# Optimization experiments

Hardware: AMD Instinct MI355X
Metric: run time of the kernel (lower is better)

The kernel has to match this reference:

```python
import jax, jax.numpy as jnp
import numpy as np

INIT_RANGE = 0.02

def setup_inputs() -> dict:
    key = jax.random.key(0)
    ks = jax.random.split(key, 5)
    B, S, D, H, Dh = 4, 2048, 768, 12, 64
    residual = jax.random.normal(ks[0], (B, S, D), dtype=jnp.float32)
    W_Q = jax.random.normal(ks[1], (H, D, Dh), dtype=jnp.float32) * INIT_RANGE
    W_K = jax.random.normal(ks[2], (H, D, Dh), dtype=jnp.float32) * INIT_RANGE
    W_V = jax.random.normal(ks[3], (H, D, Dh), dtype=jnp.float32) * INIT_RANGE
    W_O = jax.random.normal(ks[4], (H, Dh, D), dtype=jnp.float32) * INIT_RANGE
    b_Q = jnp.zeros((H, Dh), dtype=jnp.float32)
    b_K = jnp.zeros((H, Dh), dtype=jnp.float32)
    b_V = jnp.zeros((H, Dh), dtype=jnp.float32)
    b_O = jnp.zeros((D,), dtype=jnp.float32)
    return {"residual": residual, "W_Q": W_Q, "W_K": W_K, "W_V": W_V,
            "W_O": W_O, "b_Q": b_Q, "b_K": b_K, "b_V": b_V, "b_O": b_O}

def reference(residual, W_Q, W_K, W_V, W_O, b_Q, b_K, b_V, b_O):
    # residual: [b, s, d]; W_{Q,K,V}: [h, d, dh]; W_O: [h, dh, d]
    d_head = W_Q.shape[-1]
    q = jnp.einsum('bsd,hde->bshe', residual, W_Q) + b_Q  # [b, s, h, dh]
    k = jnp.einsum('bsd,hde->bshe', residual, W_K) + b_K
    v = jnp.einsum('bsd,hde->bshe', residual, W_V) + b_V
    scores = jnp.einsum('bqhe,bkhe->bhqk', q, k) / jnp.sqrt(jnp.float32(d_head))
    S = residual.shape[1]
    causal = jnp.tril(jnp.ones((S, S), dtype=bool))  # True where attending allowed
    scores = jnp.where(causal, scores, -jnp.inf)
    pattern = jax.nn.softmax(scores, axis=-1)  # [b, h, q, k]
    z = jnp.einsum('bkhe,bhqk->bqhe', v, pattern)  # [b, q, h, dh]
    attn_out = jnp.einsum('bqhe,hed->bqd', z, W_O) + b_O
    return attn_out
```

## Files before the change

kernel.cpp:

```cpp
#include <hip/hip_runtime.h>

typedef short short8 __attribute__((ext_vector_type(8)));
typedef float floatx4 __attribute__((ext_vector_type(4)));
typedef unsigned short ushort_t;


__device__ inline ushort_t f2bf(float f) {
  union { float f; unsigned u; } x; x.f = f;
  unsigned u = x.u;
  unsigned r = u + 0x7fffu + ((u >> 16) & 1u);
  return (ushort_t)(r >> 16);
}

__device__ inline unsigned pk2(float a, float b) {
  union { float f; unsigned u; } x, y; x.f = a; y.f = b;
  return ((x.u + 0x8000u) >> 16) | ((y.u + 0x8000u) & 0xffff0000u);
}

__device__ inline float fexp2(float x) {
#if __has_builtin(__builtin_amdgcn_exp2f)
  return __builtin_amdgcn_exp2f(x);
#else
  return exp2f(x);
#endif
}

__device__ inline void async16(const void* g, void* l) {
  __builtin_amdgcn_global_load_lds((const __attribute__((address_space(1))) void*)g,
                                   (__attribute__((address_space(3))) void*)l,
                                   16, 0, 0);
}


__global__ __launch_bounds__(256) void conv_rx(const float* __restrict__ x,
                                               ushort_t* __restrict__ y, int n4) {
  int i = blockIdx.x * 256 + threadIdx.x;
  if (i >= n4) return;
  float4 f = ((const float4*)x)[i];
  ushort4 o;
  o.x = f2bf(f.x); o.y = f2bf(f.y); o.z = f2bf(f.z); o.w = f2bf(f.w);
  ((ushort4*)y)[i] = o;
}

__global__ __launch_bounds__(256) void conv_w2(
    const float* __restrict__ wq, const float* __restrict__ wk, const float* __restrict__ wv,
    const float* __restrict__ wo,
    const float* __restrict__ bq, const float* __restrict__ bk, const float* __restrict__ bv,
    ushort_t* __restrict__ wqkvT, ushort_t* __restrict__ woT, float* __restrict__ bqkv)
{
  __shared__ ushort_t t[64 * 72];
  const int bid = blockIdx.x;
  const int tid = threadIdx.x;
  if (bid < 432) {
    int m = bid / 144, rem = bid % 144;
    int h = rem / 12, dt = rem % 12;
    int d0 = dt * 64;
    const float* w = (m == 0) ? wq : ((m == 1) ? wk : wv);
    const float* src = w + ((size_t)h * 768 + d0) * 64;
#pragma unroll
    for (int i = 0; i < 4; ++i) {
      int task = i * 256 + tid;
      int row = task >> 4, c4 = task & 15;
      float4 f = *(const float4*)(src + row * 64 + c4 * 4);
      ushort4 o4;
      o4.x = f2bf(f.x); o4.y = f2bf(f.y); o4.z = f2bf(f.z); o4.w = f2bf(f.w);
      *(ushort4*)&t[row * 72 + c4 * 4] = o4;
    }
    __syncthreads();
    ushort_t* dst = wqkvT + ((size_t)m * 768 + h * 64) * 768 + d0;
#pragma unroll
    for (int i = 0; i < 2; ++i) {
      int task = i * 256 + tid;
      int e = task >> 3, sc = task & 7;
      short8 d8;
#pragma unroll
      for (int j = 0; j < 8; ++j) d8[j] = (short)t[(sc * 8 + j) * 72 + e];
      *(short8*)(dst + (size_t)e * 768 + sc * 8) = d8;
    }
  } else if (bid < 576) {
    int b2 = bid - 432;
    int het = b2 / 12, dt = b2 % 12;
    int he0 = het * 64, d0 = dt * 64;
    const float* src = wo + (size_t)he0 * 768 + d0;
#pragma unroll
    for (int i = 0; i < 4; ++i) {
      int task = i * 256 + tid;
      int row = task >> 4, c4 = task & 15;
      float4 f = *(const float4*)(src + (size_t)row * 768 + c4 * 4);
      ushort4 o4;
      o4.x = f2bf(f.x); o4.y = f2bf(f.y); o4.z = f2bf(f.z); o4.w = f2bf(f.w);
      *(ushort4*)&t[row * 72 + c4 * 4] = o4;
    }
    __syncthreads();
    ushort_t* dst = woT + (size_t)d0 * 768 + he0;
#pragma unroll
    for (int i = 0; i < 2; ++i) {
      int task = i * 256 + tid;
      int dd = task >> 3, sc = task & 7;
      short8 d8;
#pragma unroll
      for (int j = 0; j < 8; ++j) d8[j] = (short)t[(sc * 8 + j) * 72 + dd];
      *(short8*)(dst + (size_t)dd * 768 + sc * 8) = d8;
    }
  } else {
    for (int idx = tid; idx < 2304; idx += 256) {
      int m = idx / 768, rem = idx - m * 768;
      const float* bp = (m == 0) ? bq : ((m == 1) ? bk : bv);
      bqkv[idx] = bp[rem];
    }
  }
}


__global__ __launch_bounds__(256) void gemm_qkv(
    const ushort_t* __restrict__ A, const ushort_t* __restrict__ Bt,
    const float* __restrict__ bias,
    ushort_t* __restrict__ q, ushort_t* __restrict__ k, ushort_t* __restrict__ v)
{
  __shared__ ushort_t lA[2][128 * 32];
  __shared__ ushort_t lB[2][128 * 32];
  const int tid = threadIdx.x;
  const int wave = tid >> 6, lane = tid & 63;
  const int ln15 = lane & 15, quad = lane >> 4;
  const int row0 = blockIdx.x * 128, col0 = blockIdx.y * 128;
  const int wm = (wave >> 1) * 64, wn = (wave & 1) * 64;
  const int c0 = wave * 2;

  const ushort_t* gA0 = A + (size_t)(row0 + c0 * 16 + (lane >> 2)) * 768 + (lane & 3) * 8;
  const ushort_t* gB0 = Bt + (size_t)(col0 + c0 * 16 + (lane >> 2)) * 768 + (lane & 3) * 8;

  floatx4 acc[4][4];
#pragma unroll
  for (int mi = 0; mi < 4; ++mi)
#pragma unroll
    for (int ni = 0; ni < 4; ++ni)
      acc[mi][ni] = (floatx4){0.f, 0.f, 0.f, 0.f};

  async16(gA0, &lA[0][c0 * 512]);
  async16(gA0 + 16 * 768, &lA[0][c0 * 512 + 512]);
  async16(gB0, &lB[0][c0 * 512]);
  async16(gB0 + 16 * 768, &lB[0][c0 * 512 + 512]);
  __syncthreads();

  for (int kt = 0; kt < 24; ++kt) {
    const int buf = kt & 1;
    if (kt + 1 < 24) {
      async16(gA0 + (kt + 1) * 32, &lA[buf ^ 1][c0 * 512]);
      async16(gA0 + (kt + 1) * 32 + 16 * 768, &lA[buf ^ 1][c0 * 512 + 512]);
      async16(gB0 + (kt + 1) * 32, &lB[buf ^ 1][c0 * 512]);
      async16(gB0 + (kt + 1) * 32 + 16 * 768, &lB[buf ^ 1][c0 * 512 + 512]);
    }
    short8 af[4], bfv[4];
#pragma unroll
    for (int mi = 0; mi < 4; ++mi)
      af[mi] = *(const short8*)&lA[buf][(wm + mi * 16 + ln15) * 32 + quad * 8];
#pragma unroll
    for (int ni = 0; ni < 4; ++ni)
      bfv[ni] = *(const short8*)&lB[buf][(wn + ni * 16 + ln15) * 32 + quad * 8];
#pragma unroll
    for (int mi = 0; mi < 4; ++mi)
#pragma unroll
      for (int ni = 0; ni < 4; ++ni)
        acc[mi][ni] = __builtin_amdgcn_mfma_f32_16x16x32_bf16(af[mi], bfv[ni], acc[mi][ni], 0, 0, 0);
    __syncthreads();
  }

  const float qscale = 0.125f * 1.44269504f;
#pragma unroll
  for (int mi = 0; mi < 4; ++mi) {
#pragma unroll
    for (int ni = 0; ni < 4; ++ni) {
      int gr = row0 + wm + mi * 16 + quad * 4;
      int gc = col0 + wn + ni * 16 + ln15;
      float bia = bias[gc];
      int m = gc / 768;
      int rem = gc - m * 768;
      int h = rem >> 6, e = rem & 63;
      ushort_t* dp = (m == 0) ? q : ((m == 1) ? k : v);
#pragma unroll
      for (int r = 0; r < 4; ++r) {
        float val = acc[mi][ni][r] + bia;
        int rr = gr + r;
        int bb = rr >> 11, ss = rr & 2047;
        size_t dst = ((size_t)((bb * 12 + h) * 2048 + ss) << 6) + e;
        dp[dst] = f2bf((m == 0) ? val * qscale : val);
      }
    }
  }
}


__global__ __launch_bounds__(256) void gemm_out(
    const ushort_t* __restrict__ A, const ushort_t* __restrict__ Bt,
    const float* __restrict__ bias, float* __restrict__ outf)
{
  __shared__ ushort_t lA[2][64 * 32];
  __shared__ ushort_t lB[2][128 * 32];
  const int tid = threadIdx.x;
  const int wave = tid >> 6, lane = tid & 63;
  const int ln15 = lane & 15, quad = lane >> 4;
  const int row0 = blockIdx.x * 64, col0 = blockIdx.y * 128;
  const int wm = (wave >> 1) * 32, wn = (wave & 1) * 64;
  const int cb = wave * 2;

  const ushort_t* gA0 = A + (size_t)(row0 + wave * 16 + (lane >> 2)) * 768 + (lane & 3) * 8;
  const ushort_t* gB0 = Bt + (size_t)(col0 + cb * 16 + (lane >> 2)) * 768 + (lane & 3) * 8;

  floatx4 acc[2][4];
#pragma unroll
  for (int mi = 0; mi < 2; ++mi)
#pragma unroll
    for (int ni = 0; ni < 4; ++ni)
      acc[mi][ni] = (floatx4){0.f, 0.f, 0.f, 0.f};

  async16(gA0, &lA[0][wave * 512]);
  async16(gB0, &lB[0][cb * 512]);
  async16(gB0 + 16 * 768, &lB[0][cb * 512 + 512]);
  __syncthreads();

  for (int kt = 0; kt < 24; ++kt) {
    const int buf = kt & 1;
    if (kt + 1 < 24) {
      async16(gA0 + (kt + 1) * 32, &lA[buf ^ 1][wave * 512]);
      async16(gB0 + (kt + 1) * 32, &lB[buf ^ 1][cb * 512]);
      async16(gB0 + (kt + 1) * 32 + 16 * 768, &lB[buf ^ 1][cb * 512 + 512]);
    }
    short8 af[2], bfv[4];
#pragma unroll
    for (int mi = 0; mi < 2; ++mi)
      af[mi] = *(const short8*)&lA[buf][(wm + mi * 16 + ln15) * 32 + quad * 8];
#pragma unroll
    for (int ni = 0; ni < 4; ++ni)
      bfv[ni] = *(const short8*)&lB[buf][(wn + ni * 16 + ln15) * 32 + quad * 8];
#pragma unroll
    for (int mi = 0; mi < 2; ++mi)
#pragma unroll
      for (int ni = 0; ni < 4; ++ni)
        acc[mi][ni] = __builtin_amdgcn_mfma_f32_16x16x32_bf16(af[mi], bfv[ni], acc[mi][ni], 0, 0, 0);
    __syncthreads();
  }

#pragma unroll
  for (int mi = 0; mi < 2; ++mi) {
#pragma unroll
    for (int ni = 0; ni < 4; ++ni) {
      int gr = row0 + wm + mi * 16 + quad * 4;
      int gc = col0 + wn + ni * 16 + ln15;
      float bia = bias[gc];
#pragma unroll
      for (int r = 0; r < 4; ++r)
        outf[(size_t)(gr + r) * 768 + gc] = acc[mi][ni][r] + bia;
    }
  }
}


__global__ __launch_bounds__(256) void transpose_v(const ushort_t* __restrict__ v,
                                                   ushort_t* __restrict__ vt)
{
  __shared__ ushort_t t[64 * 72];
  const int bh = blockIdx.y;
  const int s0 = blockIdx.x * 64;
  const ushort_t* src = v + ((size_t)bh * 2048 + s0) * 64;
#pragma unroll
  for (int t2 = 0; t2 < 2; ++t2) {
    int task = t2 * 256 + threadIdx.x;
    int row = task >> 3, ch = task & 7;
    short8 d = *(const short8*)(src + row * 64 + ch * 8);
    *(short8*)&t[row * 72 + ch * 8] = d;
  }
  __syncthreads();
  ushort_t* dst = vt + (size_t)bh * 64 * 2048 + s0;
#pragma unroll
  for (int t2 = 0; t2 < 2; ++t2) {
    int task = t2 * 256 + threadIdx.x;
    int e = task >> 3, sc = task & 7;
    short8 d;
#pragma unroll
    for (int j = 0; j < 8; ++j)
      d[j] = (short)t[(sc * 8 + j) * 72 + e];
    *(short8*)(dst + (size_t)e * 2048 + sc * 8) = d;
  }
}


__device__ inline short8 frag_ld(const ushort_t* t, int row, int ch) {
  return *(const short8*)&t[row * 64 + (((ch ^ row) & 7) * 8)];
}

__global__ __launch_bounds__(256) void attn3(
    const ushort_t* __restrict__ Q, const ushort_t* __restrict__ K,
    const ushort_t* __restrict__ VT, ushort_t* __restrict__ Z)
{
  __shared__ ushort_t lK[2][64 * 64];
  __shared__ ushort_t lV[2][64 * 64];
  __shared__ ushort_t lPQ[128 * 64];
  const int tid = threadIdx.x;
  const int wave = tid >> 6, lane = tid & 63;
  const int ln15 = lane & 15, quad = lane >> 4;
  const int bi = blockIdx.x;
  const int bh = bi % 48;
  const int t = 15 - (bi / 48);
  const int h = bh % 12, b = bh / 12;
  const size_t base = (size_t)bh * 2048 * 64;
  const ushort_t* Qp = Q + base + (size_t)t * 128 * 64;
  const ushort_t* Kp = K + base;
  const ushort_t* Vp = VT + base;
  const int nk = 2 * t + 2;

#pragma unroll
  for (int i = 0; i < 4; ++i) {
    int task = i * 256 + tid;
    int row = task >> 3, lch = task & 7;
    int c = lch ^ (row & 7);
    async16(Qp + row * 64 + c * 8, &lPQ[task * 8]);
  }
#pragma unroll
  for (int i = 0; i < 2; ++i) {
    int task = i * 256 + tid;
    int row = task >> 3, lch = task & 7;
    int c = lch ^ (row & 7);
    async16(Kp + (size_t)row * 64 + c * 8, &lK[0][task * 8]);
    async16(Vp + (size_t)row * 2048 + c * 8, &lV[0][task * 8]);
  }
  __syncthreads();
  short8 qf[2][2];
#pragma unroll
  for (int c = 0; c < 2; ++c) {
    qf[c][0] = frag_ld(lPQ, wave * 32 + c * 16 + ln15, quad);
    qf[c][1] = frag_ld(lPQ, wave * 32 + c * 16 + ln15, quad + 4);
  }
  __syncthreads();

  float l_i[2] = {0.f, 0.f};
  floatx4 o[2][4];
#pragma unroll
  for (int c = 0; c < 2; ++c)
#pragma unroll
    for (int et = 0; et < 4; ++et) o[c][et] = (floatx4){0.f, 0.f, 0.f, 0.f};

  ushort_t* lPw = lPQ + wave * 2048;
  const int qg0 = t * 128 + wave * 32 + ln15;

  for (int kt = 0; kt < nk; ++kt) {
    const int buf = kt & 1;
    if (kt + 1 < nk) {
#pragma unroll
      for (int i = 0; i < 2; ++i) {
        int task = i * 256 + tid;
        int row = task >> 3, lch = task & 7;
        int c = lch ^ (row & 7);
        async16(Kp + (size_t)((kt + 1) * 64 + row) * 64 + c * 8, &lK[buf ^ 1][task * 8]);
        async16(Vp + (size_t)row * 2048 + (kt + 1) * 64 + c * 8, &lV[buf ^ 1][task * 8]);
      }
    }

    floatx4 st[2][4];
#pragma unroll
    for (int ni = 0; ni < 4; ++ni) {
      short8 kf0 = frag_ld(lK[buf], ni * 16 + ln15, quad);
      short8 kf1 = frag_ld(lK[buf], ni * 16 + ln15, quad + 4);
#pragma unroll
      for (int c = 0; c < 2; ++c) {
        floatx4 z4 = (floatx4){0.f, 0.f, 0.f, 0.f};
        z4 = __builtin_amdgcn_mfma_f32_16x16x32_bf16(kf0, qf[c][0], z4, 0, 0, 0);
        st[c][ni] = __builtin_amdgcn_mfma_f32_16x16x32_bf16(kf1, qf[c][1], z4, 0, 0, 0);
      }
    }

    const bool masked = (kt >= 2 * t);
#pragma unroll
    for (int c = 0; c < 2; ++c) {
      const int qg = qg0 + c * 16;
      float p[16];
      float rs = 0.f;
#pragma unroll
      for (int ni = 0; ni < 4; ++ni)
#pragma unroll
        for (int r = 0; r < 4; ++r) {
          float x = st[c][ni][r];
          if (masked) {
            int kg = kt * 64 + ni * 16 + quad * 4 + r;
            x = (kg <= qg) ? x : -1e30f;
          }
          float pe = fexp2(x);
          p[ni * 4 + r] = pe;
          rs += pe;
        }
      rs += __shfl_xor(rs, 16);
      rs += __shfl_xor(rs, 32);
      l_i[c] += rs;
      const int rowl = c * 16 + ln15;
#pragma unroll
      for (int ni = 0; ni < 4; ++ni) {
        int chunk = 2 * ni + (quad >> 1);
        int pos = chunk ^ (rowl & 7);
        uint2 w;
        w.x = pk2(p[ni * 4 + 0], p[ni * 4 + 1]);
        w.y = pk2(p[ni * 4 + 2], p[ni * 4 + 3]);
        *(uint2*)&lPw[rowl * 64 + pos * 8 + (quad & 1) * 4] = w;
      }
    }

    short8 pf[2][2];
#pragma unroll
    for (int c = 0; c < 2; ++c) {
      pf[c][0] = frag_ld(lPw, c * 16 + ln15, quad);
      pf[c][1] = frag_ld(lPw, c * 16 + ln15, quad + 4);
    }
#pragma unroll
    for (int et = 0; et < 4; ++et) {
      short8 vf0 = frag_ld(lV[buf], et * 16 + ln15, quad);
      short8 vf1 = frag_ld(lV[buf], et * 16 + ln15, quad + 4);
#pragma unroll
      for (int c = 0; c < 2; ++c) {
        o[c][et] = __builtin_amdgcn_mfma_f32_16x16x32_bf16(vf0, pf[c][0], o[c][et], 0, 0, 0);
        o[c][et] = __builtin_amdgcn_mfma_f32_16x16x32_bf16(vf1, pf[c][1], o[c][et], 0, 0, 0);
      }
    }
    __syncthreads();
  }

#pragma unroll
  for (int c = 0; c < 2; ++c) {
    float inv = 1.f / l_i[c];
    size_t zrow = (size_t)(b * 2048 + t * 128 + wave * 32 + c * 16 + ln15);
#pragma unroll
    for (int et = 0; et < 4; ++et) {
      ushort4 w;
      w.x = f2bf(o[c][et][0] * inv);
      w.y = f2bf(o[c][et][1] * inv);
      w.z = f2bf(o[c][et][2] * inv);
      w.w = f2bf(o[c][et][3] * inv);
      *(ushort4*)&Z[zrow * 768 + h * 64 + et * 16 + quad * 4] = w;
    }
  }
}


extern "C" void kernel_launch(void* const* d_in, const int* in_sizes, int n_in,
                              void* d_out, int out_size, void* d_ws, size_t ws_size,
                              hipStream_t stream)
{
  const float* residual = (const float*)d_in[0];
  const float* W_Q = (const float*)d_in[1];
  const float* W_K = (const float*)d_in[2];
  const float* W_V = (const float*)d_in[3];
  const float* W_O = (const float*)d_in[4];
  const float* b_Q = (const float*)d_in[5];
  const float* b_K = (const float*)d_in[6];
  const float* b_V = (const float*)d_in[7];
  const float* b_O = (const float*)d_in[8];
  float* out = (float*)d_out;

  char* w = (char*)d_ws;
  ushort_t* rx    = (ushort_t*)(w + 0);
  ushort_t* wqkvT = (ushort_t*)(w + 12582912);
  ushort_t* woT   = (ushort_t*)(w + 16121856);
  float*    bqkv  = (float*)   (w + 17301504);
  ushort_t* q     = (ushort_t*)(w + 17310720);
  ushort_t* k     = (ushort_t*)(w + 29893632);
  ushort_t* v     = (ushort_t*)(w + 42476544);
  ushort_t* vt    = (ushort_t*)(w + 55059456);
  ushort_t* z     = rx;

  conv_rx<<<6144, 256, 0, stream>>>(residual, rx, 8192 * 768 / 4);
  conv_w2<<<577, 256, 0, stream>>>(W_Q, W_K, W_V, W_O, b_Q, b_K, b_V, wqkvT, woT, bqkv);
  gemm_qkv<<<dim3(64, 18), 256, 0, stream>>>(rx, wqkvT, bqkv, q, k, v);
  transpose_v<<<dim3(32, 48), 256, 0, stream>>>(v, vt);
  attn3<<<768, 256, 0, stream>>>(q, k, vt, z);
  gemm_out<<<dim3(128, 6), 256, 0, stream>>>(z, woT, b_O, out);
}
```

Before: 230.5 us.

## Fuse V transpose into QKV GEMM epilogue, merge conversion kernels, swizzle block order

```diff
diff --git a/kernel.cpp b/kernel.cpp
--- a/kernel.cpp
+++ b/kernel.cpp
@@ -32,25 +32,25 @@
 }
 
 
-__global__ __launch_bounds__(256) void conv_rx(const float* __restrict__ x,
-                                               ushort_t* __restrict__ y, int n4) {
-  int i = blockIdx.x * 256 + threadIdx.x;
-  if (i >= n4) return;
-  float4 f = ((const float4*)x)[i];
-  ushort4 o;
-  o.x = f2bf(f.x); o.y = f2bf(f.y); o.z = f2bf(f.z); o.w = f2bf(f.w);
-  ((ushort4*)y)[i] = o;
-}
-
-__global__ __launch_bounds__(256) void conv_w2(
+__global__ __launch_bounds__(256) void conv_prep(
+    const float* __restrict__ x, ushort_t* __restrict__ rx,
     const float* __restrict__ wq, const float* __restrict__ wk, const float* __restrict__ wv,
     const float* __restrict__ wo,
     const float* __restrict__ bq, const float* __restrict__ bk, const float* __restrict__ bv,
     ushort_t* __restrict__ wqkvT, ushort_t* __restrict__ woT, float* __restrict__ bqkv)
 {
   __shared__ ushort_t t[64 * 72];
-  const int bid = blockIdx.x;
   const int tid = threadIdx.x;
+  const int bid0 = blockIdx.x;
+  if (bid0 < 6144) {
+    int i = bid0 * 256 + tid;
+    float4 f = ((const float4*)x)[i];
+    ushort4 o;
+    o.x = f2bf(f.x); o.y = f2bf(f.y); o.z = f2bf(f.z); o.w = f2bf(f.w);
+    ((ushort4*)rx)[i] = o;
+    return;
+  }
+  const int bid = bid0 - 6144;
   if (bid < 432) {
     int m = bid / 144, rem = bid % 144;
     int h = rem / 12, dt = rem % 12;
@@ -115,14 +115,17 @@
 __global__ __launch_bounds__(256) void gemm_qkv(
     const ushort_t* __restrict__ A, const ushort_t* __restrict__ Bt,
     const float* __restrict__ bias,
-    ushort_t* __restrict__ q, ushort_t* __restrict__ k, ushort_t* __restrict__ v)
+    ushort_t* __restrict__ q, ushort_t* __restrict__ k, ushort_t* __restrict__ vt)
 {
-  __shared__ ushort_t lA[2][128 * 32];
-  __shared__ ushort_t lB[2][128 * 32];
+  __shared__ ushort_t sh[17408];
   const int tid = threadIdx.x;
   const int wave = tid >> 6, lane = tid & 63;
   const int ln15 = lane & 15, quad = lane >> 4;
-  const int row0 = blockIdx.x * 128, col0 = blockIdx.y * 128;
+  const int id = blockIdx.x;
+  const int xk = id & 7, j = id >> 3;
+  const int bx = (xk >> 1) * 16 + (j & 15);
+  const int by = (xk & 1) * 9 + (j >> 4);
+  const int row0 = bx * 128, col0 = by * 128;
   const int wm = (wave >> 1) * 64, wn = (wave & 1) * 64;
   const int c0 = wave * 2;
 
@@ -136,27 +139,31 @@
     for (int ni = 0; ni < 4; ++ni)
       acc[mi][ni] = (floatx4){0.f, 0.f, 0.f, 0.f};
 
-  async16(gA0, &lA[0][c0 * 512]);
-  async16(gA0 + 16 * 768, &lA[0][c0 * 512 + 512]);
-  async16(gB0, &lB[0][c0 * 512]);
-  async16(gB0 + 16 * 768, &lB[0][c0 * 512 + 512]);
+  async16(gA0, &sh[c0 * 512]);
+  async16(gA0 + 16 * 768, &sh[c0 * 512 + 512]);
+  async16(gB0, &sh[8192 + c0 * 512]);
+  async16(gB0 + 16 * 768, &sh[8192 + c0 * 512 + 512]);
   __syncthreads();
 
   for (int kt = 0; kt < 24; ++kt) {
     const int buf = kt & 1;
     if (kt + 1 < 24) {
-      async16(gA0 + (kt + 1) * 32, &lA[buf ^ 1][c0 * 512]);
-      async16(gA0 + (kt + 1) * 32 + 16 * 768, &lA[buf ^ 1][c0 * 512 + 512]);
-      async16(gB0 + (kt + 1) * 32, &lB[buf ^ 1][c0 * 512]);
-      async16(gB0 + (kt + 1) * 32 + 16 * 768, &lB[buf ^ 1][c0 * 512 + 512]);
-    }
+      ushort_t* dA = &sh[(buf ^ 1) * 4096];
+      ushort_t* dB = &sh[8192 + (buf ^ 1) * 4096];
+      async16(gA0 + (kt + 1) * 32, dA + c0 * 512);
+      async16(gA0 + (kt + 1) * 32 + 16 * 768, dA + c0 * 512 + 512);
+      async16(gB0 + (kt + 1) * 32, dB + c0 * 512);
+      async16(gB0 + (kt + 1) * 32 + 16 * 768, dB + c0 * 512 + 512);
+    }
+    const ushort_t* sA = &sh[buf * 4096];
+    const ushort_t* sB = &sh[8192 + buf * 4096];
     short8 af[4], bfv[4];
 #pragma unroll
     for (int mi = 0; mi < 4; ++mi)
-      af[mi] = *(const short8*)&lA[buf][(wm + mi * 16 + ln15) * 32 + quad * 8];
+      af[mi] = *(const short8*)&sA[(wm + mi * 16 + ln15) * 32 + quad * 8];
 #pragma unroll
     for (int ni = 0; ni < 4; ++ni)
-      bfv[ni] = *(const short8*)&lB[buf][(wn + ni * 16 + ln15) * 32 + quad * 8];
+      bfv[ni] = *(const short8*)&sB[(wn + ni * 16 + ln15) * 32 + quad * 8];
 #pragma unroll
     for (int mi = 0; mi < 4; ++mi)
 #pragma unroll
@@ -165,26 +172,57 @@
     __syncthreads();
   }
 
-  const float qscale = 0.125f * 1.44269504f;
-#pragma unroll
-  for (int mi = 0; mi < 4; ++mi) {
-#pragma unroll
-    for (int ni = 0; ni < 4; ++ni) {
-      int gr = row0 + wm + mi * 16 + quad * 4;
-      int gc = col0 + wn + ni * 16 + ln15;
-      float bia = bias[gc];
-      int m = gc / 768;
-      int rem = gc - m * 768;
-      int h = rem >> 6, e = rem & 63;
-      ushort_t* dp = (m == 0) ? q : ((m == 1) ? k : v);
-#pragma unroll
-      for (int r = 0; r < 4; ++r) {
-        float val = acc[mi][ni][r] + bia;
-        int rr = gr + r;
-        int bb = rr >> 11, ss = rr & 2047;
-        size_t dst = ((size_t)((bb * 12 + h) * 2048 + ss) << 6) + e;
-        dp[dst] = f2bf((m == 0) ? val * qscale : val);
+  if (col0 < 1536) {
+    const float qscale = 0.125f * 1.44269504f;
+#pragma unroll
+    for (int mi = 0; mi < 4; ++mi) {
+#pragma unroll
+      for (int ni = 0; ni < 4; ++ni) {
+        int gr = row0 + wm + mi * 16 + quad * 4;
+        int gc = col0 + wn + ni * 16 + ln15;
+        float bia = bias[gc];
+        int m = gc >> 9 >> 1;
+        m = gc / 768;
+        int rem = gc - m * 768;
+        int h = rem >> 6, e = rem & 63;
+        ushort_t* dp = (m == 0) ? q : k;
+#pragma unroll
+        for (int r = 0; r < 4; ++r) {
+          float val = acc[mi][ni][r] + bia;
+          int rr = gr + r;
+          int bb = rr >> 11, ss = rr & 2047;
+          size_t dst = ((size_t)((bb * 12 + h) * 2048 + ss) << 6) + e;
+          dp[dst] = f2bf((m == 0) ? val * qscale : val);
+        }
       }
+    }
+  } else {
+#pragma unroll
+    for (int mi = 0; mi < 4; ++mi) {
+#pragma unroll
+      for (int ni = 0; ni < 4; ++ni) {
+        int col = wn + ni * 16 + ln15;
+        int rowb = wm + mi * 16 + quad * 4;
+        float bia = bias[col0 + col];
+        ushort4 w4;
+        w4.x = f2bf(acc[mi][ni][0] + bia);
+        w4.y = f2bf(acc[mi][ni][1] + bia);
+        w4.z = f2bf(acc[mi][ni][2] + bia);
+        w4.w = f2bf(acc[mi][ni][3] + bia);
+        *(ushort4*)&sh[col * 136 + rowb] = w4;
+      }
+    }
+    __syncthreads();
+    const int relc0 = col0 - 1536;
+    const int bb = row0 >> 11, s0 = row0 & 2047;
+#pragma unroll
+    for (int i = 0; i < 8; ++i) {
+      int g = i * 256 + tid;
+      int col = g >> 4, chunk = g & 15;
+      short8 d = *(const short8*)&sh[col * 136 + chunk * 8];
+      int hh = (relc0 + col) >> 6;
+      int ee = col & 63;
+      *(short8*)(vt + (((size_t)(bb * 12 + hh) * 64 + ee) << 11) + s0 + chunk * 8) = d;
     }
   }
 }
@@ -199,7 +237,11 @@
   const int tid = threadIdx.x;
   const int wave = tid >> 6, lane = tid & 63;
   const int ln15 = lane & 15, quad = lane >> 4;
-  const int row0 = blockIdx.x * 64, col0 = blockIdx.y * 128;
+  const int id = blockIdx.x;
+  const int xk = id & 7, j = id >> 3;
+  const int bx = xk * 16 + (j & 15);
+  const int by = j >> 4;
+  const int row0 = bx * 64, col0 = by * 128;
   const int wm = (wave >> 1) * 32, wn = (wave & 1) * 64;
   const int cb = wave * 2;
 
@@ -251,35 +293,6 @@
       for (int r = 0; r < 4; ++r)
         outf[(size_t)(gr + r) * 768 + gc] = acc[mi][ni][r] + bia;
     }
-  }
-}
-
-
-__global__ __launch_bounds__(256) void transpose_v(const ushort_t* __restrict__ v,
-                                                   ushort_t* __restrict__ vt)
-{
-  __shared__ ushort_t t[64 * 72];
-  const int bh = blockIdx.y;
-  const int s0 = blockIdx.x * 64;
-  const ushort_t* src = v + ((size_t)bh * 2048 + s0) * 64;
-#pragma unroll
-  for (int t2 = 0; t2 < 2; ++t2) {
-    int task = t2 * 256 + threadIdx.x;
-    int row = task >> 3, ch = task & 7;
-    short8 d = *(const short8*)(src + row * 64 + ch * 8);
-    *(short8*)&t[row * 72 + ch * 8] = d;
-  }
-  __syncthreads();
-  ushort_t* dst = vt + (size_t)bh * 64 * 2048 + s0;
-#pragma unroll
-  for (int t2 = 0; t2 < 2; ++t2) {
-    int task = t2 * 256 + threadIdx.x;
-    int e = task >> 3, sc = task & 7;
-    short8 d;
-#pragma unroll
-    for (int j = 0; j < 8; ++j)
-      d[j] = (short)t[(sc * 8 + j) * 72 + e];
-    *(short8*)(dst + (size_t)e * 2048 + sc * 8) = d;
   }
 }
 
@@ -308,21 +321,26 @@
   const ushort_t* Vp = VT + base;
   const int nk = 2 * t + 2;
 
+  const int srow = tid >> 3, slch = tid & 7;
+  const int sc_ = slch ^ (srow & 7);
+
 #pragma unroll
   for (int i = 0; i < 4; ++i) {
     int task = i * 256 + tid;
-    int row = task >> 3, lch = task & 7;
-    int c = lch ^ (row & 7);
+    int row = task >> 3;
+    int c = slch ^ (row & 7);
     async16(Qp + row * 64 + c * 8, &lPQ[task * 8]);
   }
-#pragma unroll
-  for (int i = 0; i < 2; ++i) {
-    int task = i * 256 + tid;
-    int row = task >> 3, lch = task & 7;
-    int c = lch ^ (row & 7);
-    async16(Kp + (size_t)row * 64 + c * 8, &lK[0][task * 8]);
-    async16(Vp + (size_t)row * 2048 + c * 8, &lV[0][task * 8]);
-  }
+  async16(Kp + (size_t)srow * 64 + sc_ * 8, &lK[0][tid * 8]);
+  async16(Kp + (size_t)(srow + 32) * 64 + sc_ * 8, &lK[0][(256 + tid) * 8]);
+  async16(Vp + (size_t)srow * 2048 + sc_ * 8, &lV[0][tid * 8]);
+  async16(Vp + (size_t)(srow + 32) * 2048 + sc_ * 8, &lV[0][(256 + tid) * 8]);
+
+  const ushort_t* kPre0 = Kp + (size_t)(64 + srow) * 64 + sc_ * 8;
+  const ushort_t* kPre1 = kPre0 + 32 * 64;
+  const ushort_t* vPre0 = Vp + (size_t)srow * 2048 + 64 + sc_ * 8;
+  const ushort_t* vPre1 = vPre0 + 32 * 2048;
+
   __syncthreads();
   short8 qf[2][2];
 #pragma unroll
@@ -345,14 +363,13 @@
   for (int kt = 0; kt < nk; ++kt) {
     const int buf = kt & 1;
     if (kt + 1 < nk) {
-#pragma unroll
-      for (int i = 0; i < 2; ++i) {
-        int task = i * 256 + tid;
-        int row = task >> 3, lch = task & 7;
-        int c = lch ^ (row & 7);
-        async16(Kp + (size_t)((kt + 1) * 64 + row) * 64 + c * 8, &lK[buf ^ 1][task * 8]);
-        async16(Vp + (size_t)row * 2048 + (kt + 1) * 64 + c * 8, &lV[buf ^ 1][task * 8]);
-      }
+      ushort_t* dK = lK[buf ^ 1];
+      ushort_t* dV = lV[buf ^ 1];
+      async16(kPre0, dK + tid * 8);
+      async16(kPre1, dK + (256 + tid) * 8);
+      async16(vPre0, dV + tid * 8);
+      async16(vPre1, dV + (256 + tid) * 8);
+      kPre0 += 4096; kPre1 += 4096; vPre0 += 64; vPre1 += 64;
     }
 
     floatx4 st[2][4];
@@ -460,14 +477,12 @@
   float*    bqkv  = (float*)   (w + 17301504);
   ushort_t* q     = (ushort_t*)(w + 17310720);
   ushort_t* k     = (ushort_t*)(w + 29893632);
-  ushort_t* v     = (ushort_t*)(w + 42476544);
   ushort_t* vt    = (ushort_t*)(w + 55059456);
   ushort_t* z     = rx;
 
-  conv_rx<<<6144, 256, 0, stream>>>(residual, rx, 8192 * 768 / 4);
-  conv_w2<<<577, 256, 0, stream>>>(W_Q, W_K, W_V, W_O, b_Q, b_K, b_V, wqkvT, woT, bqkv);
-  gemm_qkv<<<dim3(64, 18), 256, 0, stream>>>(rx, wqkvT, bqkv, q, k, v);
-  transpose_v<<<dim3(32, 48), 256, 0, stream>>>(v, vt);
+  conv_prep<<<6721, 256, 0, stream>>>(residual, rx, W_Q, W_K, W_V, W_O,
+                                      b_Q, b_K, b_V, wqkvT, woT, bqkv);
+  gemm_qkv<<<1152, 256, 0, stream>>>(rx, wqkvT, bqkv, q, k, vt);
   attn3<<<768, 256, 0, stream>>>(q, k, vt, z);
-  gemm_out<<<dim3(128, 6), 256, 0, stream>>>(z, woT, b_O, out);
-}
+  gemm_out<<<768, 256, 0, stream>>>(z, woT, b_O, out);
+}
```

Result: faster. 220.0 us (-4.6%).
